# Performance work log

Measured on AMD Instinct MI355X. Metric: run time of the kernel, lower is better.

The kernel has to match this reference:

```python
import jax, jax.numpy as jnp
import numpy as np

N = 50000      # num nodes
E = 400000     # num directed edges
IN = 128       # in_channels
H = 256        # hidden_channels
OUT = 128      # out_channels
LN_EPS = 1e-5


def setup_inputs() -> dict:
    key = jax.random.key(0)
    ks = jax.random.split(key, 12)
    x = jax.random.normal(ks[0], (N, IN), jnp.float32)
    edge_index = jax.random.randint(ks[1], (2, E), 0, N, jnp.int32)

    def lin(k, fi, fo):
        return jax.random.normal(k, (fi, fo), jnp.float32) / jnp.sqrt(jnp.float32(fi))

    return {
        "x": x,
        "edge_index": edge_index,
        "W1": lin(ks[2], IN, H),  "b1": jnp.zeros((H,), jnp.float32),
        "W2": lin(ks[3], H, H),   "b2": jnp.zeros((H,), jnp.float32),
        "W3": lin(ks[4], H, H),   "b3": jnp.zeros((H,), jnp.float32),
        "W4": lin(ks[5], H, OUT), "b4": jnp.zeros((OUT,), jnp.float32),
        "g1": jnp.ones((H,), jnp.float32),   "be1": jnp.zeros((H,), jnp.float32),
        "g2": jnp.ones((H,), jnp.float32),   "be2": jnp.zeros((H,), jnp.float32),
        "g3": jnp.ones((H,), jnp.float32),   "be3": jnp.zeros((H,), jnp.float32),
        "g4": jnp.ones((OUT,), jnp.float32), "be4": jnp.zeros((OUT,), jnp.float32),
    }


def layer_norm(h, g, b):
    m = jnp.mean(h, axis=-1, keepdims=True)
    v = jnp.mean(jnp.square(h - m), axis=-1, keepdims=True)
    return (h - m) * jax.lax.rsqrt(v + LN_EPS) * g + b


def gcn_conv(h, W, b, src, dst, dinv):
    # PyG GCNConv: add self-loops, norm = deg^-1/2[src] * deg^-1/2[dst]
    h = h @ W                                             # [N, F_out]
    norm = (dinv[src] * dinv[dst])[:, None]               # [E, 1]
    msg = h[src] * norm                                   # [E, F_out] irregular gather
    agg = jax.ops.segment_sum(msg, dst, num_segments=N)   # scatter-add
    agg = agg + h * jnp.square(dinv)[:, None]             # self-loop term
    return agg + b


def reference(x, edge_index, W1, b1, W2, b2, W3, b3, W4, b4,
              g1, be1, g2, be2, g3, be3, g4, be4):
    src, dst = edge_index[0], edge_index[1]
    # degree (incl. self-loop) from destination index, as in PyG gcn_norm
    deg = jax.ops.segment_sum(jnp.ones((E,), jnp.float32), dst, num_segments=N) + 1.0
    dinv = jax.lax.rsqrt(deg)

    h = gcn_conv(x, W1, b1, src, dst, dinv)
    h = jax.nn.relu(layer_norm(h, g1, be1))   # dropout = identity (eval)
    h = gcn_conv(h, W2, b2, src, dst, dinv)
    h = jax.nn.relu(layer_norm(h, g2, be2))
    h = gcn_conv(h, W3, b3, src, dst, dinv)
    h = jax.nn.relu(layer_norm(h, g3, be3))
    h = gcn_conv(h, W4, b4, src, dst, dinv)
    h = layer_norm(h, g4, be4)
    return h
```

## Files before the change

### kernel.cpp

```cpp
#include <hip/hip_runtime.h>

#define NN 50000
#define NEDGE 400000
#define MPAD 50048
#define NB 196
constexpr float LN_EPS = 1e-5f;

typedef __attribute__((ext_vector_type(8))) short bf16x8;
typedef __attribute__((ext_vector_type(4))) float f32x4;
typedef __attribute__((ext_vector_type(8))) unsigned short ushort8v;

__device__ __forceinline__ unsigned short f2bf(float f) {
  unsigned int u = __float_as_uint(f);
  u += 0x7FFFu + ((u >> 16) & 1u);
  return (unsigned short)(u >> 16);
}
__device__ __forceinline__ float bf2f(unsigned short u) {
  return __uint_as_float(((unsigned int)u) << 16);
}

__global__ void k_count(const int* __restrict__ dst, int* __restrict__ cnt) {
  int e = blockIdx.x * blockDim.x + threadIdx.x;
  if (e < NEDGE) atomicAdd(&cnt[dst[e]], 1);
}

__global__ __launch_bounds__(256) void k_bsum(const int* __restrict__ cnt,
                                              int* __restrict__ bsum,
                                              float* __restrict__ dinv) {
  const int i = blockIdx.x * 256 + threadIdx.x;
  int v = 0;
  if (i < NN) {
    v = cnt[i];
    dinv[i] = rsqrtf((float)v + 1.0f);
  }
  int s = v;
#pragma unroll
  for (int off = 32; off > 0; off >>= 1) s += __shfl_xor(s, off);
  __shared__ int wsum[4];
  if ((threadIdx.x & 63) == 0) wsum[threadIdx.x >> 6] = s;
  __syncthreads();
  if (threadIdx.x == 0) bsum[blockIdx.x] = wsum[0] + wsum[1] + wsum[2] + wsum[3];
}

__global__ __launch_bounds__(256) void k_bscan(const int* __restrict__ bsum,
                                               int* __restrict__ boff,
                                               int* __restrict__ rowptr) {
  const int t = threadIdx.x;
  const int lane = t & 63, wid = t >> 6;
  int v = (t < NB) ? bsum[t] : 0;
  int inc = v;
  for (int off = 1; off < 64; off <<= 1) {
    int y = __shfl_up(inc, off);
    if (lane >= off) inc += y;
  }
  __shared__ int wsum[4], woff[4];
  if (lane == 63) wsum[wid] = inc;
  __syncthreads();
  if (t == 0) {
    int run = 0;
    for (int w = 0; w < 4; ++w) { woff[w] = run; run += wsum[w]; }
    rowptr[NN] = NEDGE;
  }
  __syncthreads();
  if (t < NB) boff[t] = woff[wid] + inc - v;
}

__global__ __launch_bounds__(256) void k_bapply(const int* __restrict__ cnt,
                                                const int* __restrict__ boff,
                                                int* __restrict__ rowptr) {
  const int t = threadIdx.x;
  const int i = blockIdx.x * 256 + t;
  const int lane = t & 63, wid = t >> 6;
  int v = (i < NN) ? cnt[i] : 0;
  int inc = v;
  for (int off = 1; off < 64; off <<= 1) {
    int y = __shfl_up(inc, off);
    if (lane >= off) inc += y;
  }
  __shared__ int wsum[4], woff[4];
  if (lane == 63) wsum[wid] = inc;
  __syncthreads();
  if (t == 0) {
    int run = 0;
    for (int w = 0; w < 4; ++w) { woff[w] = run; run += wsum[w]; }
  }
  __syncthreads();
  if (i < NN) rowptr[i] = boff[blockIdx.x] + woff[wid] + inc - v;
}

__global__ void k_fill(const int* __restrict__ src, const int* __restrict__ dst,
                       const float* __restrict__ dinv, const int* __restrict__ rowptr,
                       int* __restrict__ fill, int2* __restrict__ eidx2) {
  int e = blockIdx.x * blockDim.x + threadIdx.x;
  if (e >= NEDGE) return;
  const int d = dst[e];
  const int s = src[e];
  const int p = rowptr[d] + atomicAdd(&fill[d], 1);
  eidx2[p] = make_int2(s, __float_as_int(dinv[s] * dinv[d]));
}

__global__ __launch_bounds__(256) void k_wconv_all(
    const float* __restrict__ W1, const float* __restrict__ W2,
    const float* __restrict__ W3, const float* __restrict__ W4,
    unsigned short* __restrict__ Wt1, unsigned short* __restrict__ Wt2,
    unsigned short* __restrict__ Wt3, unsigned short* __restrict__ Wt4) {
  const int b = blockIdx.x;
  const int n = threadIdx.x;
  if (b < 128) {
    Wt1[(size_t)n * 128 + b] = f2bf(W1[(size_t)b * 256 + n]);
  } else if (b < 384) {
    const int k = b - 128;
    Wt2[(size_t)n * 256 + k] = f2bf(W2[(size_t)k * 256 + n]);
  } else if (b < 640) {
    const int k = b - 384;
    Wt3[(size_t)n * 256 + k] = f2bf(W3[(size_t)k * 256 + n]);
  } else {
    const int k = b - 640;
    if (n < 128) Wt4[(size_t)n * 256 + k] = f2bf(W4[(size_t)k * 128 + n]);
  }
}

__global__ void k_xconv(const float* __restrict__ in, unsigned short* __restrict__ out) {
  const int i = blockIdx.x * blockDim.x + threadIdx.x;
  if (i >= NN * 32) return;
  float4 v = reinterpret_cast<const float4*>(in)[i];
  ushort4 o; o.x = f2bf(v.x); o.y = f2bf(v.y); o.z = f2bf(v.z); o.w = f2bf(v.w);
  reinterpret_cast<ushort4*>(out)[i] = o;
}

template<int F, int NPW, int MODE>
__global__ __launch_bounds__(256) void k_gather(
    const int* __restrict__ rowptr, const int2* __restrict__ eidx2,
    const float* __restrict__ dinv, const unsigned short* __restrict__ h,
    void* __restrict__ outv, const float* __restrict__ bias,
    const float* __restrict__ gamma, const float* __restrict__ beta) {
  constexpr int LPN = 64 / NPW;
  static_assert(F / LPN == 8, "16B per lane");
  const int tid = threadIdx.x;
  const int lane = tid & 63;
  const int sub = lane / LPN;
  const int slane = lane % LPN;
  const int n = blockIdx.x * (4 * NPW) + (tid >> 6) * NPW + sub;
  const bool valid = n < NN;

  int e = 0, end = 0;
  float dn = 0.f;
  if (valid) {
    dn = dinv[n];
    e = rowptr[n];
    end = rowptr[n + 1];
  }

  float acc[8];
  ushort8v r0 = (ushort8v)0, r1 = (ushort8v)0;
  if (valid) r0 = *reinterpret_cast<const ushort8v*>(h + (size_t)n * F + slane * 8);
  const float sw = dn * dn;
#pragma unroll
  for (int j = 0; j < 8; ++j) acc[j] = bf2f(r0[j]) * sw;
  r0 = (ushort8v)0;

  while (__ballot(e < end)) {
    float w0 = 0.f, w1 = 0.f;
    if (e < end) {
      const int2 p = eidx2[e];
      w0 = __int_as_float(p.y);
      r0 = *reinterpret_cast<const ushort8v*>(h + (size_t)p.x * F + slane * 8);
    }
    if (e + 1 < end) {
      const int2 p = eidx2[e + 1];
      w1 = __int_as_float(p.y);
      r1 = *reinterpret_cast<const ushort8v*>(h + (size_t)p.x * F + slane * 8);
    }
#pragma unroll
    for (int j = 0; j < 8; ++j)
      acc[j] += w0 * bf2f(r0[j]) + w1 * bf2f(r1[j]);
    e += 2;
  }

  if (!valid) return;

  if constexpr (MODE == 0) {
    ushort8v o;
#pragma unroll
    for (int j = 0; j < 8; ++j) o[j] = f2bf(acc[j]);
    *reinterpret_cast<ushort8v*>((unsigned short*)outv + (size_t)n * F + slane * 8) = o;
  } else {
    const float4 b0 = *reinterpret_cast<const float4*>(bias + slane * 8);
    const float4 b1 = *reinterpret_cast<const float4*>(bias + slane * 8 + 4);
    acc[0] += b0.x; acc[1] += b0.y; acc[2] += b0.z; acc[3] += b0.w;
    acc[4] += b1.x; acc[5] += b1.y; acc[6] += b1.z; acc[7] += b1.w;
    float s = 0.f, q = 0.f;
#pragma unroll
    for (int j = 0; j < 8; ++j) { s += acc[j]; q = fmaf(acc[j], acc[j], q); }
#pragma unroll
    for (int off = 1; off < 16; off <<= 1) {
      s += __shfl_xor(s, off);
      q += __shfl_xor(q, off);
    }
    const float mean = s * (1.0f / 128.0f);
    const float var = q * (1.0f / 128.0f) - mean * mean;
    const float inv = rsqrtf(var + LN_EPS);
    const float4 g0 = *reinterpret_cast<const float4*>(gamma + slane * 8);
    const float4 g1 = *reinterpret_cast<const float4*>(gamma + slane * 8 + 4);
    const float4 e0 = *reinterpret_cast<const float4*>(beta + slane * 8);
    const float4 e1 = *reinterpret_cast<const float4*>(beta + slane * 8 + 4);
    float4 o0, o1;
    o0.x = (acc[0] - mean) * inv * g0.x + e0.x;
    o0.y = (acc[1] - mean) * inv * g0.y + e0.y;
    o0.z = (acc[2] - mean) * inv * g0.z + e0.z;
    o0.w = (acc[3] - mean) * inv * g0.w + e0.w;
    o1.x = (acc[4] - mean) * inv * g1.x + e1.x;
    o1.y = (acc[5] - mean) * inv * g1.y + e1.y;
    o1.z = (acc[6] - mean) * inv * g1.z + e1.z;
    o1.w = (acc[7] - mean) * inv * g1.w + e1.w;
    float* out = (float*)outv + (size_t)n * 128 + slane * 8;
    *reinterpret_cast<float4*>(out) = o0;
    *reinterpret_cast<float4*>(out + 4) = o1;
  }
}

template<int K, int N, bool LNFUSE>
__global__ __launch_bounds__(256) void k_mgemm(const unsigned short* __restrict__ A,
                                               const unsigned short* __restrict__ Bt,
                                               const float* __restrict__ bias,
                                               const float* __restrict__ gamma,
                                               const float* __restrict__ beta,
                                               unsigned short* __restrict__ out) {
  constexpr int NT = N / 64;
  constexpr int KS = K / 32;
  __shared__ __align__(16) unsigned short As[64 * K];

  const int tid = threadIdx.x;
  const int lane = tid & 63;
  const int w = tid >> 6;
  const int m0 = blockIdx.x * 64;

#pragma unroll
  for (int i = 0; i < KS; ++i) {
    const int o = (i * 256 + tid) * 16;
    const int row = o / (2 * K);
    const int inb = o % (2 * K);
    uint4 val = *reinterpret_cast<const uint4*>(
        (const char*)A + (size_t)(m0 + row) * (2 * K) + inb);
    const int dsto = o ^ ((row & 7) << 4);
    *reinterpret_cast<uint4*>((char*)As + dsto) = val;
  }
  __syncthreads();

  f32x4 acc[4][NT];
#pragma unroll
  for (int mt = 0; mt < 4; ++mt)
#pragma unroll
    for (int nt = 0; nt < NT; ++nt) acc[mt][nt] = (f32x4){0.f, 0.f, 0.f, 0.f};

  const int nw0 = w * (N / 4);
  const int arow = lane & 15;
  const int kgrp = (lane >> 4) * 8;

  for (int ks = 0; ks < KS; ++ks) {
    bf16x8 af[4];
#pragma unroll
    for (int mt = 0; mt < 4; ++mt) {
      const int r = mt * 16 + arow;
      int boff = (r * K + ks * 32 + kgrp) * 2;
      boff ^= (r & 7) << 4;
      af[mt] = *reinterpret_cast<const bf16x8*>((const char*)As + boff);
    }
    bf16x8 bfr[NT];
#pragma unroll
    for (int nt = 0; nt < NT; ++nt) {
      const int n = nw0 + nt * 16 + arow;
      bfr[nt] = *reinterpret_cast<const bf16x8*>(Bt + (size_t)n * K + ks * 32 + kgrp);
    }
#pragma unroll
    for (int mt = 0; mt < 4; ++mt)
#pragma unroll
      for (int nt = 0; nt < NT; ++nt)
        acc[mt][nt] = __builtin_amdgcn_mfma_f32_16x16x32_bf16(af[mt], bfr[nt], acc[mt][nt], 0, 0, 0);
  }

  const int g = lane >> 4;
  const int cl = lane & 15;

  if constexpr (LNFUSE) {
    float gv[NT], bev[NT];
#pragma unroll
    for (int nt = 0; nt < NT; ++nt) {
      const int c = nw0 + nt * 16 + cl;
      const float bv = bias[c];
      gv[nt] = gamma[c];
      bev[nt] = beta[c];
#pragma unroll
      for (int mt = 0; mt < 4; ++mt)
#pragma unroll
        for (int reg = 0; reg < 4; ++reg) acc[mt][nt][reg] += bv;
    }
    __shared__ float sS[4][64];
    __shared__ float sQ[4][64];
    float ps[4][4], pq[4][4];
#pragma unroll
    for (int mt = 0; mt < 4; ++mt) {
#pragma unroll
      for (int reg = 0; reg < 4; ++reg) {
        float s = 0.f, q = 0.f;
#pragma unroll
        for (int nt = 0; nt < NT; ++nt) {
          const float v = acc[mt][nt][reg];
          s += v; q = fmaf(v, v, q);
        }
#pragma unroll
        for (int off = 1; off < 16; off <<= 1) {
          s += __shfl_xor(s, off);
          q += __shfl_xor(q, off);
        }
        ps[mt][reg] = s; pq[mt][reg] = q;
      }
    }
    if (cl == 0) {
#pragma unroll
      for (int mt = 0; mt < 4; ++mt)
#pragma unroll
        for (int reg = 0; reg < 4; ++reg) {
          sS[w][mt * 16 + g * 4 + reg] = ps[mt][reg];
          sQ[w][mt * 16 + g * 4 + reg] = pq[mt][reg];
        }
    }
    __syncthreads();
#pragma unroll
    for (int mt = 0; mt < 4; ++mt) {
#pragma unroll
      for (int reg = 0; reg < 4; ++reg) {
        const int rr = mt * 16 + g * 4 + reg;
        const int r = m0 + rr;
        const float S = sS[0][rr] + sS[1][rr] + sS[2][rr] + sS[3][rr];
        const float Q = sQ[0][rr] + sQ[1][rr] + sQ[2][rr] + sQ[3][rr];
        const float mean = S * (1.0f / N);
        const float var = Q * (1.0f / N) - mean * mean;
        const float inv = rsqrtf(var + LN_EPS);
        if (r < NN) {
#pragma unroll
          for (int nt = 0; nt < NT; ++nt) {
            const int c = nw0 + nt * 16 + cl;
            const float o = fmaxf((acc[mt][nt][reg] - mean) * inv * gv[nt] + bev[nt], 0.f);
            out[(size_t)r * N + c] = f2bf(o);
          }
        }
      }
    }
  } else {
#pragma unroll
    for (int mt = 0; mt < 4; ++mt) {
#pragma unroll
      for (int nt = 0; nt < NT; ++nt) {
        const int c = nw0 + nt * 16 + cl;
#pragma unroll
        for (int reg = 0; reg < 4; ++reg) {
          const int r = m0 + mt * 16 + g * 4 + reg;
          if (r < NN) out[(size_t)r * N + c] = f2bf(acc[mt][nt][reg]);
        }
      }
    }
  }
}

extern "C" void kernel_launch(void* const* d_in, const int* in_sizes, int n_in,
                              void* d_out, int out_size, void* d_ws, size_t ws_size,
                              hipStream_t stream) {
  const float* x   = (const float*)d_in[0];
  const int*   ei  = (const int*)d_in[1];
  const float* W1  = (const float*)d_in[2];
  const float* b1  = (const float*)d_in[3];
  const float* W2  = (const float*)d_in[4];
  const float* b2  = (const float*)d_in[5];
  const float* W3  = (const float*)d_in[6];
  const float* b3  = (const float*)d_in[7];
  const float* W4  = (const float*)d_in[8];
  const float* b4  = (const float*)d_in[9];
  const float* g1  = (const float*)d_in[10];
  const float* be1 = (const float*)d_in[11];
  const float* g2  = (const float*)d_in[12];
  const float* be2 = (const float*)d_in[13];
  const float* g3  = (const float*)d_in[14];
  const float* be3 = (const float*)d_in[15];
  const float* g4  = (const float*)d_in[16];
  const float* be4 = (const float*)d_in[17];

  const int* src = ei;
  const int* dst = ei + NEDGE;

  char* ws = (char*)d_ws;
  int*   cnt    = (int*)(ws + 0);
  int*   fill   = (int*)(ws + 204800);
  int*   rowptr = (int*)(ws + 409600);
  float* dinv   = (float*)(ws + 614400);
  int*   bsum   = (int*)(ws + 819200);
  int*   boff   = (int*)(ws + 823296);
  int2*  eidx2  = (int2*)(ws + 827392);
  unsigned short* Wt1 = (unsigned short*)(ws + 4030464);
  unsigned short* Wt2 = (unsigned short*)(ws + 4096000);
  unsigned short* Wt3 = (unsigned short*)(ws + 4227072);
  unsigned short* Wt4 = (unsigned short*)(ws + 4358144);
  unsigned short* xB  = (unsigned short*)(ws + 4423680);
  unsigned short* aggB = (unsigned short*)(ws + 17235968);
  unsigned short* hB   = (unsigned short*)(ws + 42860544);
  unsigned short* t4B  = (unsigned short*)(ws + 68485120);
  float* out = (float*)d_out;

  const int MB = (NN + 63) / 64;

  hipMemsetAsync(cnt, 0, 409600, stream);
  k_count<<<(NEDGE + 255) / 256, 256, 0, stream>>>(dst, cnt);
  k_bsum<<<NB, 256, 0, stream>>>(cnt, bsum, dinv);
  k_bscan<<<1, 256, 0, stream>>>(bsum, boff, rowptr);
  k_bapply<<<NB, 256, 0, stream>>>(cnt, boff, rowptr);
  k_fill<<<(NEDGE + 255) / 256, 256, 0, stream>>>(src, dst, dinv, rowptr, fill, eidx2);
  k_wconv_all<<<896, 256, 0, stream>>>(W1, W2, W3, W4, Wt1, Wt2, Wt3, Wt4);
  k_xconv<<<(NN * 32 + 255) / 256, 256, 0, stream>>>(x, xB);

  k_gather<128, 4, 0><<<(NN + 15) / 16, 256, 0, stream>>>(rowptr, eidx2, dinv, xB, aggB, nullptr, nullptr, nullptr);
  k_mgemm<128, 256, true><<<MB, 256, 0, stream>>>(aggB, Wt1, b1, g1, be1, hB);

  k_gather<256, 2, 0><<<(NN + 7) / 8, 256, 0, stream>>>(rowptr, eidx2, dinv, hB, aggB, nullptr, nullptr, nullptr);
  k_mgemm<256, 256, true><<<MB, 256, 0, stream>>>(aggB, Wt2, b2, g2, be2, hB);

  k_gather<256, 2, 0><<<(NN + 7) / 8, 256, 0, stream>>>(rowptr, eidx2, dinv, hB, aggB, nullptr, nullptr, nullptr);
  k_mgemm<256, 256, true><<<MB, 256, 0, stream>>>(aggB, Wt3, b3, g3, be3, hB);

  k_mgemm<256, 128, false><<<MB, 256, 0, stream>>>(hB, Wt4, nullptr, nullptr, nullptr, t4B);
  k_gather<128, 4, 1><<<(NN + 15) / 16, 256, 0, stream>>>(rowptr, eidx2, dinv, t4B, out, b4, g4, be4);
}
```

Measured before the change: 297.8 us.

## Merge preprocessing kernels, fold block scan into apply, unroll gather by four

Weight conversion, x conversion and count zeroing move into one k_prep launch, which replaces the memset and two kernels. The single-block scan is folded into k_bapply, where every block redundantly scans the block sums in shared memory. k_bapply now writes a cursor array so k_fill needs one atomic per edge instead of an atomic plus a rowptr read. The gather loop handles four edges per iteration instead of two, to raise memory-level parallelism at the cost of more registers.

```diff
diff --git a/kernel.cpp b/kernel.cpp
--- a/kernel.cpp
+++ b/kernel.cpp
@@ -19,91 +19,13 @@
   return __uint_as_float(((unsigned int)u) << 16);
 }
 
-__global__ void k_count(const int* __restrict__ dst, int* __restrict__ cnt) {
-  int e = blockIdx.x * blockDim.x + threadIdx.x;
-  if (e < NEDGE) atomicAdd(&cnt[dst[e]], 1);
-}
-
-__global__ __launch_bounds__(256) void k_bsum(const int* __restrict__ cnt,
-                                              int* __restrict__ bsum,
-                                              float* __restrict__ dinv) {
-  const int i = blockIdx.x * 256 + threadIdx.x;
-  int v = 0;
-  if (i < NN) {
-    v = cnt[i];
-    dinv[i] = rsqrtf((float)v + 1.0f);
-  }
-  int s = v;
-#pragma unroll
-  for (int off = 32; off > 0; off >>= 1) s += __shfl_xor(s, off);
-  __shared__ int wsum[4];
-  if ((threadIdx.x & 63) == 0) wsum[threadIdx.x >> 6] = s;
-  __syncthreads();
-  if (threadIdx.x == 0) bsum[blockIdx.x] = wsum[0] + wsum[1] + wsum[2] + wsum[3];
-}
-
-__global__ __launch_bounds__(256) void k_bscan(const int* __restrict__ bsum,
-                                               int* __restrict__ boff,
-                                               int* __restrict__ rowptr) {
-  const int t = threadIdx.x;
-  const int lane = t & 63, wid = t >> 6;
-  int v = (t < NB) ? bsum[t] : 0;
-  int inc = v;
-  for (int off = 1; off < 64; off <<= 1) {
-    int y = __shfl_up(inc, off);
-    if (lane >= off) inc += y;
-  }
-  __shared__ int wsum[4], woff[4];
-  if (lane == 63) wsum[wid] = inc;
-  __syncthreads();
-  if (t == 0) {
-    int run = 0;
-    for (int w = 0; w < 4; ++w) { woff[w] = run; run += wsum[w]; }
-    rowptr[NN] = NEDGE;
-  }
-  __syncthreads();
-  if (t < NB) boff[t] = woff[wid] + inc - v;
-}
-
-__global__ __launch_bounds__(256) void k_bapply(const int* __restrict__ cnt,
-                                                const int* __restrict__ boff,
-                                                int* __restrict__ rowptr) {
-  const int t = threadIdx.x;
-  const int i = blockIdx.x * 256 + t;
-  const int lane = t & 63, wid = t >> 6;
-  int v = (i < NN) ? cnt[i] : 0;
-  int inc = v;
-  for (int off = 1; off < 64; off <<= 1) {
-    int y = __shfl_up(inc, off);
-    if (lane >= off) inc += y;
-  }
-  __shared__ int wsum[4], woff[4];
-  if (lane == 63) wsum[wid] = inc;
-  __syncthreads();
-  if (t == 0) {
-    int run = 0;
-    for (int w = 0; w < 4; ++w) { woff[w] = run; run += wsum[w]; }
-  }
-  __syncthreads();
-  if (i < NN) rowptr[i] = boff[blockIdx.x] + woff[wid] + inc - v;
-}
-
-__global__ void k_fill(const int* __restrict__ src, const int* __restrict__ dst,
-                       const float* __restrict__ dinv, const int* __restrict__ rowptr,
-                       int* __restrict__ fill, int2* __restrict__ eidx2) {
-  int e = blockIdx.x * blockDim.x + threadIdx.x;
-  if (e >= NEDGE) return;
-  const int d = dst[e];
-  const int s = src[e];
-  const int p = rowptr[d] + atomicAdd(&fill[d], 1);
-  eidx2[p] = make_int2(s, __float_as_int(dinv[s] * dinv[d]));
-}
-
-__global__ __launch_bounds__(256) void k_wconv_all(
+__global__ __launch_bounds__(256) void k_prep(
     const float* __restrict__ W1, const float* __restrict__ W2,
     const float* __restrict__ W3, const float* __restrict__ W4,
     unsigned short* __restrict__ Wt1, unsigned short* __restrict__ Wt2,
-    unsigned short* __restrict__ Wt3, unsigned short* __restrict__ Wt4) {
+    unsigned short* __restrict__ Wt3, unsigned short* __restrict__ Wt4,
+    const float* __restrict__ x, unsigned short* __restrict__ xB,
+    int* __restrict__ cnt) {
   const int b = blockIdx.x;
   const int n = threadIdx.x;
   if (b < 128) {
@@ -114,18 +36,101 @@
   } else if (b < 640) {
     const int k = b - 384;
     Wt3[(size_t)n * 256 + k] = f2bf(W3[(size_t)k * 256 + n]);
-  } else {
+  } else if (b < 896) {
     const int k = b - 640;
     if (n < 128) Wt4[(size_t)n * 256 + k] = f2bf(W4[(size_t)k * 128 + n]);
-  }
-}
-
-__global__ void k_xconv(const float* __restrict__ in, unsigned short* __restrict__ out) {
-  const int i = blockIdx.x * blockDim.x + threadIdx.x;
-  if (i >= NN * 32) return;
-  float4 v = reinterpret_cast<const float4*>(in)[i];
-  ushort4 o; o.x = f2bf(v.x); o.y = f2bf(v.y); o.z = f2bf(v.z); o.w = f2bf(v.w);
-  reinterpret_cast<ushort4*>(out)[i] = o;
+  } else if (b < 7146) {
+    const int i = (b - 896) * 256 + n;
+    float4 v = reinterpret_cast<const float4*>(x)[i];
+    ushort4 o; o.x = f2bf(v.x); o.y = f2bf(v.y); o.z = f2bf(v.z); o.w = f2bf(v.w);
+    reinterpret_cast<ushort4*>(xB)[i] = o;
+  } else {
+    const int i = (b - 7146) * 256 + n;
+    if (i < NN) cnt[i] = 0;
+  }
+}
+
+__global__ void k_count(const int* __restrict__ dst, int* __restrict__ cnt) {
+  int e = blockIdx.x * blockDim.x + threadIdx.x;
+  if (e < NEDGE) atomicAdd(&cnt[dst[e]], 1);
+}
+
+__global__ __launch_bounds__(256) void k_bsum(const int* __restrict__ cnt,
+                                              int* __restrict__ bsum,
+                                              float* __restrict__ dinv) {
+  const int i = blockIdx.x * 256 + threadIdx.x;
+  int v = 0;
+  if (i < NN) {
+    v = cnt[i];
+    dinv[i] = rsqrtf((float)v + 1.0f);
+  }
+  int s = v;
+#pragma unroll
+  for (int off = 32; off > 0; off >>= 1) s += __shfl_xor(s, off);
+  __shared__ int wsum[4];
+  if ((threadIdx.x & 63) == 0) wsum[threadIdx.x >> 6] = s;
+  __syncthreads();
+  if (threadIdx.x == 0) bsum[blockIdx.x] = wsum[0] + wsum[1] + wsum[2] + wsum[3];
+}
+
+__global__ __launch_bounds__(256) void k_bapply(const int* __restrict__ cnt,
+                                                const int* __restrict__ bsum,
+                                                int* __restrict__ rowptr,
+                                                int* __restrict__ cursor) {
+  __shared__ int sOff[NB];
+  __shared__ int wsum[4], woff[4];
+  const int t = threadIdx.x;
+  const int lane = t & 63, wid = t >> 6;
+
+  {
+    int v = (t < NB) ? bsum[t] : 0;
+    int inc = v;
+    for (int off = 1; off < 64; off <<= 1) {
+      int y = __shfl_up(inc, off);
+      if (lane >= off) inc += y;
+    }
+    if (lane == 63) wsum[wid] = inc;
+    __syncthreads();
+    if (t == 0) {
+      int run = 0;
+      for (int w = 0; w < 4; ++w) { woff[w] = run; run += wsum[w]; }
+    }
+    __syncthreads();
+    if (t < NB) sOff[t] = woff[wid] + inc - v;
+  }
+  __syncthreads();
+
+  const int i = blockIdx.x * 256 + t;
+  int v = (i < NN) ? cnt[i] : 0;
+  int inc = v;
+  for (int off = 1; off < 64; off <<= 1) {
+    int y = __shfl_up(inc, off);
+    if (lane >= off) inc += y;
+  }
+  if (lane == 63) wsum[wid] = inc;
+  __syncthreads();
+  if (t == 0) {
+    int run = 0;
+    for (int w = 0; w < 4; ++w) { woff[w] = run; run += wsum[w]; }
+  }
+  __syncthreads();
+  if (i < NN) {
+    const int rp = sOff[blockIdx.x] + woff[wid] + inc - v;
+    rowptr[i] = rp;
+    cursor[i] = rp;
+  }
+  if (blockIdx.x == 0 && t == 0) rowptr[NN] = NEDGE;
+}
+
+__global__ void k_fill(const int* __restrict__ src, const int* __restrict__ dst,
+                       const float* __restrict__ dinv, int* __restrict__ cursor,
+                       int2* __restrict__ eidx2) {
+  int e = blockIdx.x * blockDim.x + threadIdx.x;
+  if (e >= NEDGE) return;
+  const int d = dst[e];
+  const int s = src[e];
+  const int p = atomicAdd(&cursor[d], 1);
+  eidx2[p] = make_int2(s, __float_as_int(dinv[s] * dinv[d]));
 }
 
 template<int F, int NPW, int MODE>
@@ -152,7 +157,7 @@
   }
 
   float acc[8];
-  ushort8v r0 = (ushort8v)0, r1 = (ushort8v)0;
+  ushort8v r0 = (ushort8v)0, r1 = (ushort8v)0, r2 = (ushort8v)0, r3 = (ushort8v)0;
   if (valid) r0 = *reinterpret_cast<const ushort8v*>(h + (size_t)n * F + slane * 8);
   const float sw = dn * dn;
 #pragma unroll
@@ -160,7 +165,7 @@
   r0 = (ushort8v)0;
 
   while (__ballot(e < end)) {
-    float w0 = 0.f, w1 = 0.f;
+    float w0 = 0.f, w1 = 0.f, w2 = 0.f, w3 = 0.f;
     if (e < end) {
       const int2 p = eidx2[e];
       w0 = __int_as_float(p.y);
@@ -171,10 +176,20 @@
       w1 = __int_as_float(p.y);
       r1 = *reinterpret_cast<const ushort8v*>(h + (size_t)p.x * F + slane * 8);
     }
+    if (e + 2 < end) {
+      const int2 p = eidx2[e + 2];
+      w2 = __int_as_float(p.y);
+      r2 = *reinterpret_cast<const ushort8v*>(h + (size_t)p.x * F + slane * 8);
+    }
+    if (e + 3 < end) {
+      const int2 p = eidx2[e + 3];
+      w3 = __int_as_float(p.y);
+      r3 = *reinterpret_cast<const ushort8v*>(h + (size_t)p.x * F + slane * 8);
+    }
 #pragma unroll
     for (int j = 0; j < 8; ++j)
-      acc[j] += w0 * bf2f(r0[j]) + w1 * bf2f(r1[j]);
-    e += 2;
+      acc[j] += w0 * bf2f(r0[j]) + w1 * bf2f(r1[j]) + w2 * bf2f(r2[j]) + w3 * bf2f(r3[j]);
+    e += 4;
   }
 
   if (!valid) return;
@@ -390,11 +405,10 @@
 
   char* ws = (char*)d_ws;
   int*   cnt    = (int*)(ws + 0);
-  int*   fill   = (int*)(ws + 204800);
+  int*   cursor = (int*)(ws + 204800);
   int*   rowptr = (int*)(ws + 409600);
   float* dinv   = (float*)(ws + 614400);
   int*   bsum   = (int*)(ws + 819200);
-  int*   boff   = (int*)(ws + 823296);
   int2*  eidx2  = (int2*)(ws + 827392);
   unsigned short* Wt1 = (unsigned short*)(ws + 4030464);
   unsigned short* Wt2 = (unsigned short*)(ws + 4096000);
@@ -408,14 +422,11 @@
 
   const int MB = (NN + 63) / 64;
 
-  hipMemsetAsync(cnt, 0, 409600, stream);
+  k_prep<<<7342, 256, 0, stream>>>(W1, W2, W3, W4, Wt1, Wt2, Wt3, Wt4, x, xB, cnt);
   k_count<<<(NEDGE + 255) / 256, 256, 0, stream>>>(dst, cnt);
   k_bsum<<<NB, 256, 0, stream>>>(cnt, bsum, dinv);
-  k_bscan<<<1, 256, 0, stream>>>(bsum, boff, rowptr);
-  k_bapply<<<NB, 256, 0, stream>>>(cnt, boff, rowptr);
-  k_fill<<<(NEDGE + 255) / 256, 256, 0, stream>>>(src, dst, dinv, rowptr, fill, eidx2);
-  k_wconv_all<<<896, 256, 0, stream>>>(W1, W2, W3, W4, Wt1, Wt2, Wt3, Wt4);
-  k_xconv<<<(NN * 32 + 255) / 256, 256, 0, stream>>>(x, xB);
+  k_bapply<<<NB, 256, 0, stream>>>(cnt, bsum, rowptr, cursor);
+  k_fill<<<(NEDGE + 255) / 256, 256, 0, stream>>>(src, dst, dinv, cursor, eidx2);
 
   k_gather<128, 4, 0><<<(NN + 15) / 16, 256, 0, stream>>>(rowptr, eidx2, dinv, xB, aggB, nullptr, nullptr, nullptr);
   k_mgemm<128, 256, true><<<MB, 256, 0, stream>>>(aggB, Wt1, b1, g1, be1, hB);
```

Measured after the change: 285.3 us. -4.2%, faster.
